# Kernel tuning notes

Hardware: AMD Instinct MI355X
Metric: run time of the kernel (lower is better)

## Reference

```python
import jax, jax.numpy as jnp
import numpy as np

L, C, B = 256, 20, 1024


def _pos_mask(L):
    # pairwise mask: l2 - l1 >= 1, shape (L, L); broadcast over channels
    ls = jnp.arange(L)
    return (ls[None, :] - ls[:, None]) >= 1


def setup_inputs() -> dict:
    key = jax.random.key(0)
    k0, k1, k2 = jax.random.split(key, 3)
    x_lc = jax.random.uniform(k0, (B, L, C), dtype=jnp.float32)
    theta_0 = jnp.zeros((1,), dtype=jnp.float32)
    theta_lc = jax.random.normal(k1, (1, L, C), dtype=jnp.float32) / np.sqrt(L)
    pm = _pos_mask(L)
    theta_lclc = (jax.random.normal(k2, (1, L, C, L, C), dtype=jnp.float32)
                  / np.sqrt(L * L)) * pm[None, :, None, :, None]
    mask = pm
    return {"x_lc": x_lc, "theta_0": theta_0, "theta_lc": theta_lc,
            "theta_lclc": theta_lclc, "mask": mask}


def reference(x_lc, theta_0, theta_lc, theta_lclc, mask):
    Bn = x_lc.shape[0]
    # additive term: sum_{l,c} theta_lc * x
    phi = theta_0 + jnp.einsum('blc,zlc->b', x_lc, theta_lc)[:, None]
    # pairwise term as a masked bilinear form: x^T (mask * theta) x
    # (avoids materializing the (B,L,C,L,C) broadcast of the original)
    theta_m = theta_lclc[0] * mask[:, None, :, None].astype(theta_lclc.dtype)
    LC = L * C
    xf = x_lc.reshape(Bn, LC)                      # (B, LC)
    tf_ = theta_m.reshape(LC, LC)                  # (LC, LC)
    pair = jnp.einsum('bi,ij,bj->b', xf, tf_, xf)  # two GEMMs under the hood
    phi = phi + pair[:, None]
    return phi
```

## Files before the change

### kernel.cpp

```cpp
#include <hip/hip_runtime.h>
#include <stdint.h>

#define LDIM 256
#define CDIM 20
#define LC   5120
#define NB   1024
#define BM   256
#define BN   256
#define ITOT64 840

typedef __attribute__((ext_vector_type(8))) short short8;
typedef __attribute__((ext_vector_type(4))) float float4v;
typedef __attribute__((ext_vector_type(4))) unsigned int uint4v;
typedef unsigned short ushort_t;

#define TB_BYTES (52428800ull)
#define XB_BYTES (10485760ull)
#define WS_NEED  (TB_BYTES + XB_BYTES)

__device__ inline uint32_t pack_bf16x2(float a, float b) {
    uint32_t ua = __float_as_uint(a);
    uint32_t ub = __float_as_uint(b);
    ua += 0x7fffu + ((ua >> 16) & 1u);
    ub += 0x7fffu + ((ub >> 16) & 1u);
    return (ua >> 16) | (ub & 0xffff0000u);
}

__device__ inline float bf16_to_f32(ushort_t u) {
    return __uint_as_float(((uint32_t)u) << 16);
}

__device__ inline void load_lds16(const void* g, void* l) {
    __builtin_amdgcn_global_load_lds(
        (const __attribute__((address_space(1))) uint32_t*)g,
        (__attribute__((address_space(3))) uint32_t*)l, 16, 0, 0);
}

__global__ __launch_bounds__(256) void conv_kernel(
    const float* __restrict__ T, const float* __restrict__ X,
    const float* __restrict__ th0, const float* __restrict__ thlc,
    ushort_t* __restrict__ Tb, ushort_t* __restrict__ Xb,
    float* __restrict__ out)
{
    const int bid = blockIdx.x;
    const int t   = threadIdx.x;
    __shared__ float red[4];

    if (bid < LC) {
        const int r  = bid;
        const int tk = (r >> 8) << 8;
        const float*  src = T  + (size_t)r * LC;
        ushort_t*     dst = Tb + (size_t)r * LC;
        for (int c = tk + t * 4; c < LC; c += 1024) {
            float4 f = *(const float4*)(src + c);
            uint2 u;
            u.x = pack_bf16x2(f.x, f.y);
            u.y = pack_bf16x2(f.z, f.w);
            *(uint2*)(dst + c) = u;
        }
    } else {
        const int b = bid - LC;
        const float*  src = X  + (size_t)b * LC;
        ushort_t*     dst = Xb + (size_t)b * LC;
        float s = 0.f;
        for (int c = t * 4; c < LC; c += 1024) {
            float4 f = *(const float4*)(src + c);
            float4 w = *(const float4*)(thlc + c);
            s += f.x * w.x + f.y * w.y + f.z * w.z + f.w * w.w;
            uint2 u;
            u.x = pack_bf16x2(f.x, f.y);
            u.y = pack_bf16x2(f.z, f.w);
            *(uint2*)(dst + c) = u;
        }
        s += __shfl_xor(s, 1);  s += __shfl_xor(s, 2);  s += __shfl_xor(s, 4);
        s += __shfl_xor(s, 8);  s += __shfl_xor(s, 16); s += __shfl_xor(s, 32);
        if ((t & 63) == 0) red[t >> 6] = s;
        __syncthreads();
        if (t == 0) out[b] = th0[0] + red[0] + red[1] + red[2] + red[3];
    }
}

__global__ __launch_bounds__(512, 2) void pair_bf(
    const ushort_t* __restrict__ Tb, const ushort_t* __restrict__ Xb,
    float* __restrict__ out)
{
    const int n    = blockIdx.x;
    const int kblk = (n & 7) | ((n >> 5) << 3);
    const int bn0  = ((n >> 3) & 3) * BN;

    const int gbeg = (ITOT64 * kblk) >> 6;
    const int gend = (ITOT64 * (kblk + 1)) >> 6;

    int it = 0, pre = 0;
    while (pre + (80 - (it << 2)) <= gbeg) { pre += 80 - (it << 2); ++it; }
    const int li = gbeg - pre;

    __shared__ __align__(16) ushort_t A_s[2][2048 * 8];
    __shared__ __align__(16) ushort_t B_s[2][2048 * 8];

    const int t    = threadIdx.x;
    const int lane = t & 63;
    const int wid  = t >> 6;
    const int wm   = (wid >> 1) * 64;
    const int wn   = (wid & 1) * 128;
    const int l16  = lane & 15;
    const int qk   = lane >> 4;

    uint32_t offA[4], offB[4];
    #pragma unroll
    for (int j = 0; j < 4; ++j) {
        const int c = (wid << 8) + (j << 6) + lane;
        const int row = c >> 3;
        const int g = (c & 7) ^ (row & 7);
        offA[j] = (uint32_t)row * LC + (g << 3);
        offB[j] = (uint32_t)(bn0 + row) * LC + (g << 3);
    }

    int adrA[2][4], adrB[2][8];
    #pragma unroll
    for (int step = 0; step < 2; ++step) {
        const int kf = step * 4 + qk;
        #pragma unroll
        for (int mt = 0; mt < 4; ++mt) {
            const int r = wm + mt * 16 + l16;
            adrA[step][mt] = ((r << 3) + (kf ^ (r & 7))) << 4;
        }
        #pragma unroll
        for (int nt = 0; nt < 8; ++nt) {
            const int r = wn + nt * 16 + l16;
            adrB[step][nt] = ((r << 3) + (kf ^ (r & 7))) << 4;
        }
    }

    int itI = it, liI = li;
    int k0; size_t baseA;
    auto rebaseI = [&]() {
        const int i0I = itI << 8;
        k0    = i0I + (liI << 6);
        baseA = (size_t)i0I * LC + k0;
    };
    rebaseI();
    auto issue = [&](int cb) {
        #pragma unroll
        for (int j = 0; j < 4; ++j)
            load_lds16(Tb + baseA + offA[j], A_s[cb] + (((wid << 8) + (j << 6)) << 3));
        #pragma unroll
        for (int j = 0; j < 4; ++j)
            load_lds16(Xb + k0 + offB[j],   B_s[cb] + (((wid << 8) + (j << 6)) << 3));
        ++liI;
        if (liI == 80 - (itI << 2)) {
            ++itI; liI = 0;
            if (itI < 20) rebaseI();
        } else { k0 += 64; baseA += 64; }
    };

    float4v acc[4][8];
    #pragma unroll
    for (int mt = 0; mt < 4; ++mt)
        #pragma unroll
        for (int nt = 0; nt < 8; ++nt)
            #pragma unroll
            for (int r = 0; r < 4; ++r) acc[mt][nt][r] = 0.f;

    int itC = it, liC = li;

    issue(0);

    for (int g = gbeg; g < gend; ++g) {
        const int cur = (g - gbeg) & 1;
        __syncthreads();
        if (g + 1 < gend) issue(cur ^ 1);

        {
            const ushort_t* As = A_s[cur];
            const ushort_t* Bs = B_s[cur];
            #pragma unroll
            for (int step = 0; step < 2; ++step) {
                short8 af[4], bfr[8];
                #pragma unroll
                for (int mt = 0; mt < 4; ++mt)
                    af[mt] = *(const short8*)((const char*)As + adrA[step][mt]);
                #pragma unroll
                for (int nt = 0; nt < 8; ++nt)
                    bfr[nt] = *(const short8*)((const char*)Bs + adrB[step][nt]);
                #pragma unroll
                for (int mt = 0; mt < 4; ++mt)
                    #pragma unroll
                    for (int nt = 0; nt < 8; ++nt)
                        acc[mt][nt] = __builtin_amdgcn_mfma_f32_16x16x32_bf16(
                            af[mt], bfr[nt], acc[mt][nt], 0, 0, 0);
            }
        }

        ++liC;
        const bool segEnd = (liC == 80 - (itC << 2));
        if (segEnd || g + 1 == gend) {
            const int i0 = itC << 8;
            #pragma unroll
            for (int nt = 0; nt < 8; ++nt) {
                const int b = bn0 + wn + nt * 16 + l16;
                const ushort_t* xb = Xb + (size_t)b * LC + i0 + wm + qk * 4;
                float s = 0.f;
                #pragma unroll
                for (int mt = 0; mt < 4; ++mt) {
                    ushort4 xv = *(const ushort4*)(xb + mt * 16);
                    s += acc[mt][nt][0] * bf16_to_f32(xv.x)
                       + acc[mt][nt][1] * bf16_to_f32(xv.y)
                       + acc[mt][nt][2] * bf16_to_f32(xv.z)
                       + acc[mt][nt][3] * bf16_to_f32(xv.w);
                }
                s += __shfl_xor(s, 16);
                s += __shfl_xor(s, 32);
                if (qk == 0) atomicAdd(&out[b], s);
            }
            #pragma unroll
            for (int mt = 0; mt < 4; ++mt)
                #pragma unroll
                for (int nt = 0; nt < 8; ++nt)
                    #pragma unroll
                    for (int r = 0; r < 4; ++r) acc[mt][nt][r] = 0.f;
        }
        if (segEnd) { ++itC; liC = 0; }
    }
}

__global__ __launch_bounds__(256) void init_kernel(
    const float* __restrict__ x, const float* __restrict__ th0,
    const float* __restrict__ thlc, float* __restrict__ out)
{
    const int b = blockIdx.x;
    const float4* xb = (const float4*)(x + (size_t)b * LC);
    const float4* tv = (const float4*)thlc;
    float s = 0.f;
    for (int i = threadIdx.x; i < LC / 4; i += 256) {
        float4 a = xb[i], t = tv[i];
        s += a.x * t.x + a.y * t.y + a.z * t.z + a.w * t.w;
    }
    s += __shfl_xor(s, 1);  s += __shfl_xor(s, 2);  s += __shfl_xor(s, 4);
    s += __shfl_xor(s, 8);  s += __shfl_xor(s, 16); s += __shfl_xor(s, 32);
    __shared__ float red[4];
    if ((threadIdx.x & 63) == 0) red[threadIdx.x >> 6] = s;
    __syncthreads();
    if (threadIdx.x == 0) out[b] = th0[0] + red[0] + red[1] + red[2] + red[3];
}

__global__ __launch_bounds__(256) void pair_kernel(
    const float* __restrict__ T, const float* __restrict__ X,
    float* __restrict__ out)
{
    const int n  = blockIdx.x;
    const int r  = n & 7;
    const int g  = n >> 3;
    const int i0  = (g >> 3) * 128;
    const int bn0 = (g & 7) * 128;
    const int kstart = i0;
    const int nIter  = (LC - kstart) >> 6;
    const int ipc    = (nIter + 7) >> 3;
    const int itBeg  = r * ipc;
    const int itEnd  = (itBeg + ipc < nIter) ? (itBeg + ipc) : nIter;
    if (itBeg >= itEnd) return;
    const int kbeg   = kstart + (itBeg << 6);

    __shared__ __align__(16) short A_s[8 * 128 * 8];
    __shared__ __align__(16) short B_s[8 * 128 * 8];

    const int t    = threadIdx.x;
    const int lane = t & 63;
    const int wid  = t >> 6;
    const int wm   = (wid >> 1) * 64;
    const int wn   = (wid & 1) * 64;
    const int l16  = lane & 15;
    const int qk   = lane >> 4;

    const float* pA[4]; const float* pB[4]; int sIdx[4];
    #pragma unroll
    for (int u = 0; u < 4; ++u) {
        const int id  = t + u * 256;
        const int row = id >> 3;
        const int kq  = id & 7;
        pA[u] = T + (size_t)(i0 + row) * LC + kbeg + kq * 8;
        pB[u] = X + (size_t)(bn0 + row) * LC + kbeg + kq * 8;
        sIdx[u] = (kq * 128 + (row ^ kq)) * 8;
    }

    float4v acc[4][4] = {};
    for (int itr = itBeg; itr < itEnd; ++itr) {
        __syncthreads();
        #pragma unroll
        for (int u = 0; u < 4; ++u) {
            float4 a0 = ((const float4*)pA[u])[0];
            float4 a1 = ((const float4*)pA[u])[1];
            float4 b0 = ((const float4*)pB[u])[0];
            float4 b1 = ((const float4*)pB[u])[1];
            pA[u] += 64; pB[u] += 64;
            uint4v va, vb;
            va[0] = pack_bf16x2(a0.x, a0.y); va[1] = pack_bf16x2(a0.z, a0.w);
            va[2] = pack_bf16x2(a1.x, a1.y); va[3] = pack_bf16x2(a1.z, a1.w);
            vb[0] = pack_bf16x2(b0.x, b0.y); vb[1] = pack_bf16x2(b0.z, b0.w);
            vb[2] = pack_bf16x2(b1.x, b1.y); vb[3] = pack_bf16x2(b1.z, b1.w);
            *(uint4v*)(A_s + sIdx[u]) = va;
            *(uint4v*)(B_s + sIdx[u]) = vb;
        }
        __syncthreads();
        #pragma unroll
        for (int step = 0; step < 2; ++step) {
            const int kf = step * 4 + qk;
            short8 af[4], bfr[4];
            #pragma unroll
            for (int mt = 0; mt < 4; ++mt)
                af[mt] = *(const short8*)(A_s + (kf * 128 + ((wm + mt * 16 + l16) ^ kf)) * 8);
            #pragma unroll
            for (int nt = 0; nt < 4; ++nt)
                bfr[nt] = *(const short8*)(B_s + (kf * 128 + ((wn + nt * 16 + l16) ^ kf)) * 8);
            #pragma unroll
            for (int mt = 0; mt < 4; ++mt)
                #pragma unroll
                for (int nt = 0; nt < 4; ++nt)
                    acc[mt][nt] = __builtin_amdgcn_mfma_f32_16x16x32_bf16(
                        af[mt], bfr[nt], acc[mt][nt], 0, 0, 0);
        }
    }
    #pragma unroll
    for (int nt = 0; nt < 4; ++nt) {
        const int b = bn0 + wn + nt * 16 + l16;
        const float* xb = X + (size_t)b * LC + i0 + wm + qk * 4;
        float s = 0.f;
        #pragma unroll
        for (int mt = 0; mt < 4; ++mt) {
            float4 xv = *(const float4*)(xb + mt * 16);
            s += acc[mt][nt][0] * xv.x + acc[mt][nt][1] * xv.y +
                 acc[mt][nt][2] * xv.z + acc[mt][nt][3] * xv.w;
        }
        s += __shfl_xor(s, 16);
        s += __shfl_xor(s, 32);
        if (qk == 0) atomicAdd(&out[b], s);
    }
}

extern "C" void kernel_launch(void* const* d_in, const int* in_sizes, int n_in,
                              void* d_out, int out_size, void* d_ws, size_t ws_size,
                              hipStream_t stream) {
    const float* x    = (const float*)d_in[0];
    const float* th0  = (const float*)d_in[1];
    const float* thlc = (const float*)d_in[2];
    const float* T    = (const float*)d_in[3];
    float* out = (float*)d_out;

    if (ws_size >= WS_NEED) {
        ushort_t* Tb = (ushort_t*)d_ws;
        ushort_t* Xb = (ushort_t*)((char*)d_ws + TB_BYTES);
        conv_kernel<<<LC + NB, 256, 0, stream>>>(T, x, th0, thlc, Tb, Xb, out);
        pair_bf<<<256, 512, 0, stream>>>(Tb, Xb, out);
    } else {
        init_kernel<<<NB, 256, 0, stream>>>(x, th0, thlc, out);
        pair_kernel<<<(LC / 128) * (NB / 128) * 8, 256, 0, stream>>>(T, x, out);
    }
}
```

Measured before the change: 217.6 us.

## Restructure bf16 pair GEMM to 1024 threads, K=32 stages with fragment prefetch

After: 220.6 us. About the same (+1.4%).

```diff
diff --git a/kernel.cpp b/kernel.cpp
--- a/kernel.cpp
+++ b/kernel.cpp
@@ -7,7 +7,7 @@
 #define NB   1024
 #define BM   256
 #define BN   256
-#define ITOT64 840
+#define ITOT32 1680
 
 typedef __attribute__((ext_vector_type(8))) short short8;
 typedef __attribute__((ext_vector_type(4))) float float4v;
@@ -80,7 +80,7 @@
     }
 }
 
-__global__ __launch_bounds__(512, 2) void pair_bf(
+__global__ __launch_bounds__(1024, 4) void pair_bf(
     const ushort_t* __restrict__ Tb, const ushort_t* __restrict__ Xb,
     float* __restrict__ out)
 {
@@ -88,116 +88,100 @@
     const int kblk = (n & 7) | ((n >> 5) << 3);
     const int bn0  = ((n >> 3) & 3) * BN;
 
-    const int gbeg = (ITOT64 * kblk) >> 6;
-    const int gend = (ITOT64 * (kblk + 1)) >> 6;
+    const int gbeg = (ITOT32 * kblk) >> 6;
+    const int gend = (ITOT32 * (kblk + 1)) >> 6;
 
     int it = 0, pre = 0;
-    while (pre + (80 - (it << 2)) <= gbeg) { pre += 80 - (it << 2); ++it; }
+    while (pre + (160 - (it << 3)) <= gbeg) { pre += 160 - (it << 3); ++it; }
     const int li = gbeg - pre;
 
-    __shared__ __align__(16) ushort_t A_s[2][2048 * 8];
-    __shared__ __align__(16) ushort_t B_s[2][2048 * 8];
+    __shared__ __align__(16) ushort_t A_s[2][1024 * 8];
+    __shared__ __align__(16) ushort_t B_s[2][1024 * 8];
 
     const int t    = threadIdx.x;
     const int lane = t & 63;
     const int wid  = t >> 6;
-    const int wm   = (wid >> 1) * 64;
-    const int wn   = (wid & 1) * 128;
+    const int wm   = (wid & 3) * 64;
+    const int wn   = (wid >> 2) * 64;
     const int l16  = lane & 15;
     const int qk   = lane >> 4;
 
-    uint32_t offA[4], offB[4];
-    #pragma unroll
-    for (int j = 0; j < 4; ++j) {
-        const int c = (wid << 8) + (j << 6) + lane;
-        const int row = c >> 3;
-        const int g = (c & 7) ^ (row & 7);
-        offA[j] = (uint32_t)row * LC + (g << 3);
-        offB[j] = (uint32_t)(bn0 + row) * LC + (g << 3);
-    }
-
-    int adrA[2][4], adrB[2][8];
-    #pragma unroll
-    for (int step = 0; step < 2; ++step) {
-        const int kf = step * 4 + qk;
-        #pragma unroll
-        for (int mt = 0; mt < 4; ++mt) {
-            const int r = wm + mt * 16 + l16;
-            adrA[step][mt] = ((r << 3) + (kf ^ (r & 7))) << 4;
-        }
-        #pragma unroll
-        for (int nt = 0; nt < 8; ++nt) {
-            const int r = wn + nt * 16 + l16;
-            adrB[step][nt] = ((r << 3) + (kf ^ (r & 7))) << 4;
-        }
+    const int  cch = (wid << 6) + lane;
+    const int  rw  = cch >> 2;
+    const int  gA  = (cch & 3) ^ ((rw ^ (rw >> 2)) & 3);
+    const uint32_t offA = (uint32_t)rw * LC + (gA << 3);
+    const uint32_t offB = (uint32_t)(bn0 + rw) * LC + (gA << 3);
+    const int  ldsW = wid << 9;
+
+    int adrA[4], adrB[4];
+    #pragma unroll
+    for (int mt = 0; mt < 4; ++mt) {
+        const int r = wm + mt * 16 + l16;
+        adrA[mt] = ((r << 2) + (qk ^ ((r ^ (r >> 2)) & 3))) << 4;
+    }
+    #pragma unroll
+    for (int nt = 0; nt < 4; ++nt) {
+        const int r = wn + nt * 16 + l16;
+        adrB[nt] = ((r << 2) + (qk ^ ((r ^ (r >> 2)) & 3))) << 4;
     }
 
     int itI = it, liI = li;
-    int k0; size_t baseA;
+    uint32_t k0, baseA;
     auto rebaseI = [&]() {
-        const int i0I = itI << 8;
-        k0    = i0I + (liI << 6);
-        baseA = (size_t)i0I * LC + k0;
+        const uint32_t i0I = itI << 8;
+        k0    = i0I + (liI << 5);
+        baseA = i0I * LC + k0;
     };
     rebaseI();
     auto issue = [&](int cb) {
-        #pragma unroll
-        for (int j = 0; j < 4; ++j)
-            load_lds16(Tb + baseA + offA[j], A_s[cb] + (((wid << 8) + (j << 6)) << 3));
-        #pragma unroll
-        for (int j = 0; j < 4; ++j)
-            load_lds16(Xb + k0 + offB[j],   B_s[cb] + (((wid << 8) + (j << 6)) << 3));
+        load_lds16(Tb + baseA + offA, A_s[cb] + ldsW);
+        load_lds16(Xb + k0   + offB, B_s[cb] + ldsW);
         ++liI;
-        if (liI == 80 - (itI << 2)) {
+        if (liI == 160 - (itI << 3)) {
             ++itI; liI = 0;
             if (itI < 20) rebaseI();
-        } else { k0 += 64; baseA += 64; }
+        } else { k0 += 32; baseA += 32; }
     };
 
-    float4v acc[4][8];
+    float4v acc[4][4];
     #pragma unroll
     for (int mt = 0; mt < 4; ++mt)
         #pragma unroll
-        for (int nt = 0; nt < 8; ++nt)
+        for (int nt = 0; nt < 4; ++nt)
             #pragma unroll
             for (int r = 0; r < 4; ++r) acc[mt][nt][r] = 0.f;
 
     int itC = it, liC = li;
 
     issue(0);
+    issue(1);
+    __syncthreads();
+    short8 fa[4], fb[4];
+    #pragma unroll
+    for (int mt = 0; mt < 4; ++mt)
+        fa[mt] = *(const short8*)((const char*)A_s[0] + adrA[mt]);
+    #pragma unroll
+    for (int nt = 0; nt < 4; ++nt)
+        fb[nt] = *(const short8*)((const char*)B_s[0] + adrB[nt]);
 
     for (int g = gbeg; g < gend; ++g) {
         const int cur = (g - gbeg) & 1;
         __syncthreads();
-        if (g + 1 < gend) issue(cur ^ 1);
-
-        {
-            const ushort_t* As = A_s[cur];
-            const ushort_t* Bs = B_s[cur];
-            #pragma unroll
-            for (int step = 0; step < 2; ++step) {
-                short8 af[4], bfr[8];
-                #pragma unroll
-                for (int mt = 0; mt < 4; ++mt)
-                    af[mt] = *(const short8*)((const char*)As + adrA[step][mt]);
-                #pragma unroll
-                for (int nt = 0; nt < 8; ++nt)
-                    bfr[nt] = *(const short8*)((const char*)Bs + adrB[step][nt]);
-                #pragma unroll
-                for (int mt = 0; mt < 4; ++mt)
-                    #pragma unroll
-                    for (int nt = 0; nt < 8; ++nt)
-                        acc[mt][nt] = __builtin_amdgcn_mfma_f32_16x16x32_bf16(
-                            af[mt], bfr[nt], acc[mt][nt], 0, 0, 0);
-            }
-        }
+        if (g + 2 < gend) issue(cur);
+
+        #pragma unroll
+        for (int mt = 0; mt < 4; ++mt)
+            #pragma unroll
+            for (int nt = 0; nt < 4; ++nt)
+                acc[mt][nt] = __builtin_amdgcn_mfma_f32_16x16x32_bf16(
+                    fa[mt], fb[nt], acc[mt][nt], 0, 0, 0);
 
         ++liC;
-        const bool segEnd = (liC == 80 - (itC << 2));
+        const bool segEnd = (liC == 160 - (itC << 3));
         if (segEnd || g + 1 == gend) {
             const int i0 = itC << 8;
             #pragma unroll
-            for (int nt = 0; nt < 8; ++nt) {
+            for (int nt = 0; nt < 4; ++nt) {
                 const int b = bn0 + wn + nt * 16 + l16;
                 const ushort_t* xb = Xb + (size_t)b * LC + i0 + wm + qk * 4;
                 float s = 0.f;
@@ -216,11 +200,22 @@
             #pragma unroll
             for (int mt = 0; mt < 4; ++mt)
                 #pragma unroll
-                for (int nt = 0; nt < 8; ++nt)
+                for (int nt = 0; nt < 4; ++nt)
                     #pragma unroll
                     for (int r = 0; r < 4; ++r) acc[mt][nt][r] = 0.f;
         }
         if (segEnd) { ++itC; liC = 0; }
+
+        if (g + 1 < gend) {
+            const char* As = (const char*)A_s[cur ^ 1];
+            const char* Bs = (const char*)B_s[cur ^ 1];
+            #pragma unroll
+            for (int mt = 0; mt < 4; ++mt)
+                fa[mt] = *(const short8*)(As + adrA[mt]);
+            #pragma unroll
+            for (int nt = 0; nt < 4; ++nt)
+                fb[nt] = *(const short8*)(Bs + adrB[nt]);
+        }
     }
 }
 
@@ -350,7 +345,7 @@
         ushort_t* Tb = (ushort_t*)d_ws;
         ushort_t* Xb = (ushort_t*)((char*)d_ws + TB_BYTES);
         conv_kernel<<<LC + NB, 256, 0, stream>>>(T, x, th0, thlc, Tb, Xb, out);
-        pair_bf<<<256, 512, 0, stream>>>(Tb, Xb, out);
+        pair_bf<<<256, 1024, 0, stream>>>(Tb, Xb, out);
     } else {
         init_kernel<<<NB, 256, 0, stream>>>(x, th0, thlc, out);
         pair_kernel<<<(LC / 128) * (NB / 128) * 8, 256, 0, stream>>>(T, x, out);
```
